# Kernel tuning notes

Measured on AMD Instinct MI355X. Metric: run time of the kernel, lower is better.

The kernel has to match this reference:

```python
import jax, jax.numpy as jnp
import numpy as np

# ---- hyperparameters (from init_kwargs) ----
B, SEQ, D_MODEL = 2, 2048, 1024
D_STATE, D_CONV, EXPAND, HEAD_DIM, CHUNK = 128, 4, 2, 64, 256
D_INNER = EXPAND * D_MODEL            # 2048
NH = D_INNER // HEAD_DIM              # 32 heads
CONV_DIM = D_INNER + 2 * D_STATE      # 2304
D_IN_PROJ = 2 * D_INNER + 2 * D_STATE + NH  # z, xBC, dt -> 4384
D_FF = 4 * D_MODEL
EPS = 1e-12


def setup_inputs() -> dict:
    key = jax.random.key(0)
    ks = jax.random.split(key, 16)
    s = 0.02
    f32 = jnp.float32
    inp = {
        "x": jax.random.normal(ks[0], (B, SEQ, D_MODEL), f32),
        "time_diff": jax.random.uniform(ks[1], (B, SEQ), f32),
        # TiSSD (Mamba2-style) params
        "W_in": jax.random.normal(ks[2], (D_MODEL, D_IN_PROJ), f32) * s,
        "b_in": jnp.zeros((D_IN_PROJ,), f32),
        "conv_w": jax.random.normal(ks[3], (CONV_DIM, D_CONV), f32) * s,
        "conv_b": jnp.zeros((CONV_DIM,), f32),
        "A_log": jnp.log(jnp.arange(1, NH + 1, dtype=f32)),
        "dt_bias": jnp.full((NH,), -2.0, f32),
        "D": jnp.ones((NH,), f32),
        "time_decay": jnp.full((NH,), -3.0, f32),   # time-aware decay rates
        "rms_w": jnp.ones((D_INNER,), f32),
        "W_out": jax.random.normal(ks[4], (D_INNER, D_MODEL), f32) * s,
        "b_out": jnp.zeros((D_MODEL,), f32),
        # wrapper LayerNorm
        "ln_g": jnp.ones((D_MODEL,), f32),
        "ln_b": jnp.zeros((D_MODEL,), f32),
        # FFN
        "fc1_w": jax.random.normal(ks[5], (D_MODEL, D_FF), f32) * s,
        "fc1_b": jnp.zeros((D_FF,), f32),
        "fc2_w": jax.random.normal(ks[6], (D_FF, D_MODEL), f32) * s,
        "fc2_b": jnp.zeros((D_MODEL,), f32),
        "ln2_g": jnp.ones((D_MODEL,), f32),
        "ln2_b": jnp.zeros((D_MODEL,), f32),
    }
    return inp


def _layer_norm(x, g, b, eps=EPS):
    mu = jnp.mean(x, axis=-1, keepdims=True)
    var = jnp.mean(jnp.square(x - mu), axis=-1, keepdims=True)
    return (x - mu) * jax.lax.rsqrt(var + eps) * g + b


def _hardswish(x):
    return x * jnp.clip(x + 3.0, 0.0, 6.0) * (1.0 / 6.0)


def _tissd_forward(x, time_diff, W_in, b_in, conv_w, conv_b, A_log, dt_bias, D,
                   time_decay, rms_w, W_out, b_out):
    b, l, _ = x.shape
    zxbcdt = x @ W_in + b_in                       # [b,l,D_IN_PROJ]
    z = zxbcdt[..., :D_INNER]
    xBC = zxbcdt[..., D_INNER:D_INNER + CONV_DIM]
    dt_raw = zxbcdt[..., -NH:]

    # causal depthwise conv1d (small fixed kernel -> unrolled shifts)
    xp = jnp.pad(xBC, ((0, 0), (D_CONV - 1, 0), (0, 0)))
    xBC_c = conv_b
    for k in range(D_CONV):
        xBC_c = xBC_c + xp[:, k:k + l, :] * conv_w[:, k]
    xBC_c = jax.nn.silu(xBC_c)

    xs = xBC_c[..., :D_INNER]
    Bm = xBC_c[..., D_INNER:D_INNER + D_STATE]     # [b,l,n]
    Cm = xBC_c[..., -D_STATE:]                     # [b,l,n]

    dt = jax.nn.softplus(dt_raw + dt_bias)         # [b,l,h]
    A = -jnp.exp(A_log)                            # [h]
    # time-aware: extra decay proportional to time gap
    dA = dt * A - jax.nn.softplus(time_decay) * time_diff[..., None]  # [b,l,h]

    xh = xs.reshape(b, l, NH, HEAD_DIM)
    xdt = xh * dt[..., None]                       # [b,l,h,p]

    nc = l // CHUNK
    xc = xdt.reshape(b, nc, CHUNK, NH, HEAD_DIM)
    Bc = Bm.reshape(b, nc, CHUNK, D_STATE)
    Cc = Cm.reshape(b, nc, CHUNK, D_STATE)
    dAc = dA.reshape(b, nc, CHUNK, NH).transpose(0, 3, 1, 2)  # [b,h,c,L]

    A_cum = jnp.cumsum(dAc, axis=-1)               # [b,h,c,L]
    seg = A_cum[..., :, None] - A_cum[..., None, :]
    mask = jnp.tril(jnp.ones((CHUNK, CHUNK), bool))
    Lmat = jnp.where(mask, jnp.exp(jnp.where(mask, seg, 0.0)), 0.0)  # [b,h,c,L,L]

    # intra-chunk (diagonal block) output
    Y_diag = jnp.einsum("bcln,bcsn,bhcls,bcshp->bclhp", Cc, Bc, Lmat, xc)

    # per-chunk final states
    decay_states = jnp.exp(A_cum[..., -1:] - A_cum)  # [b,h,c,L]
    states = jnp.einsum("bcln,bhcl,bclhp->bchpn", Bc, decay_states, xc)
    chunk_decay = jnp.exp(A_cum[..., -1])            # [b,h,c]

    # inter-chunk recurrence over nc chunks
    states_t = states.transpose(1, 0, 2, 3, 4)       # [c,b,h,p,n]
    decay_t = chunk_decay.transpose(2, 0, 1)         # [c,b,h]

    def step(carry, inp):
        s_c, d_c = inp
        new = carry * d_c[..., None, None] + s_c
        return new, carry                            # emit state BEFORE chunk

    init = jnp.zeros((b, NH, HEAD_DIM, D_STATE), x.dtype)
    _, prev_states = jax.lax.scan(step, init, (states_t, decay_t))
    prev_states = prev_states.transpose(1, 0, 2, 3, 4)  # [b,c,h,p,n]

    state_decay = jnp.exp(A_cum)                     # [b,h,c,L]
    Y_off = jnp.einsum("bcln,bchpn,bhcl->bclhp", Cc, prev_states, state_decay)

    Y = (Y_diag + Y_off).reshape(b, l, NH, HEAD_DIM) + D[None, None, :, None] * xh
    y = Y.reshape(b, l, D_INNER)

    # gated RMSNorm
    y = y * jax.nn.silu(z)
    y = y * jax.lax.rsqrt(jnp.mean(jnp.square(y), axis=-1, keepdims=True) + EPS) * rms_w
    return y @ W_out + b_out


def reference(x, time_diff, W_in, b_in, conv_w, conv_b, A_log, dt_bias, D,
              time_decay, rms_w, W_out, b_out, ln_g, ln_b,
              fc1_w, fc1_b, fc2_w, fc2_b, ln2_g, ln2_b):
    hidden = _tissd_forward(x, time_diff, W_in, b_in, conv_w, conv_b, A_log,
                            dt_bias, D, time_decay, rms_w, W_out, b_out)
    # num_layers > 1 -> residual; dropout is identity in eval mode
    h = _layer_norm(hidden + x, ln_g, ln_b)
    # FFN with Hardswish and residual LayerNorm
    hid = _hardswish(h @ fc1_w + fc1_b)
    hid = hid @ fc2_w + fc2_b
    out = _layer_norm(hid + h, ln2_g, ln2_b)
    return (out, time_diff)
```

## Files before the change

### kernel.cpp

```cpp
#include <hip/hip_runtime.h>

#define BATCH 2
#define SEQL 2048
#define DM 1024
#define DSTATE 128
#define HD 64
#define CHUNK 256
#define DI 2048
#define NHEADS 32
#define CONVD 2304
#define DPROJ 4384
#define DPROJ_PAD 4608
#define DFF 4096
#define NC 8
#define ROWS (BATCH*SEQL)

typedef unsigned short ushort_t;
typedef short bf16x8 __attribute__((ext_vector_type(8)));
typedef float f32x4 __attribute__((ext_vector_type(4)));

__device__ __forceinline__ float softplus_f(float v){
    return (v > 20.f) ? v : log1pf(expf(v));
}
__device__ __forceinline__ float silu_f(float v){
    return v / (1.f + expf(-v));
}
__device__ __forceinline__ ushort_t f2b(float v){
    union { float f; unsigned int u; } x; x.f = v;
    unsigned int r = x.u + 0x7fffu + ((x.u >> 16) & 1u);
    return (ushort_t)(r >> 16);
}
__device__ __forceinline__ float b2f(ushort_t v){
    union { unsigned int u; float f; } x; x.u = ((unsigned int)v) << 16;
    return x.f;
}

template<int ACT, int OUT_BF16, int TN, int NS, int DTX>
__global__ __launch_bounds__(256) void mfma_gemm_k(
    const ushort_t* __restrict__ A, const ushort_t* __restrict__ Bt,
    const float* __restrict__ bias, float* __restrict__ Cf,
    ushort_t* __restrict__ Cb, float* __restrict__ dtaux,
    int M, int N, int K, int ldc)
{
    constexpr int NT = (TN == 128) ? 4 : 2;
    constexpr int BROWS = TN / 4;
    __shared__ ushort_t As[128*64];
    __shared__ ushort_t Bs[TN*64];
    int tid = threadIdx.x;
    int lane = tid & 63, wave = tid >> 6;
    int m0 = blockIdx.y * 128, n0 = blockIdx.x * TN;
    int Ks = K / NS;
    int kb = (NS > 1) ? blockIdx.z * Ks : 0;
    int wave_m = (TN==128) ? (wave >> 1)*64 : (wave & 1)*64;
    int wave_n = (TN==128) ? (wave & 1)*64 : (wave >> 1)*32;
    int lrow = lane >> 3;
    int lcol = ((lane & 7) ^ lrow) * 8;
    const ushort_t* Abase = A  + (size_t)(m0 + wave*32    + lrow)*K + lcol + kb;
    const ushort_t* Bbase = Bt + (size_t)(n0 + wave*BROWS + lrow)*K + lcol + kb;
    ushort_t* AsW = &As[(wave*32)*64];
    ushort_t* BsW = &Bs[(wave*BROWS)*64];
    f32x4 acc[4][NT];
    #pragma unroll
    for (int i=0;i<4;i++)
        #pragma unroll
        for (int j=0;j<NT;j++) acc[i][j] = (f32x4){0.f,0.f,0.f,0.f};
    int lm = lane & 15;
    int quad = lane >> 4;
    for (int k0 = 0; k0 < Ks; k0 += 64){
        #pragma unroll
        for (int j = 0; j < 4; j++)
            __builtin_amdgcn_global_load_lds(
                (const __attribute__((address_space(1))) void*)(Abase + (size_t)(j*8)*K + k0),
                (__attribute__((address_space(3))) void*)(AsW + j*8*64), 16, 0, 0);
        #pragma unroll
        for (int j = 0; j < BROWS/8; j++)
            __builtin_amdgcn_global_load_lds(
                (const __attribute__((address_space(1))) void*)(Bbase + (size_t)(j*8)*K + k0),
                (__attribute__((address_space(3))) void*)(BsW + j*8*64), 16, 0, 0);
        __syncthreads();
        #pragma unroll
        for (int kk = 0; kk < 64; kk += 32){
            int cb = kk >> 3;
            bf16x8 af[4], bfr[NT];
            #pragma unroll
            for (int mt=0; mt<4; mt++)
                af[mt] = *(const bf16x8*)&As[(wave_m + mt*16 + lm)*64 + (((cb + quad) ^ (lm & 7))*8)];
            #pragma unroll
            for (int nt=0; nt<NT; nt++)
                bfr[nt] = *(const bf16x8*)&Bs[(wave_n + nt*16 + lm)*64 + (((cb + quad) ^ (lm & 7))*8)];
            #pragma unroll
            for (int mt=0; mt<4; mt++)
                #pragma unroll
                for (int nt=0; nt<NT; nt++)
                    acc[mt][nt] = __builtin_amdgcn_mfma_f32_16x16x32_bf16(af[mt], bfr[nt], acc[mt][nt], 0, 0, 0);
        }
        __syncthreads();
    }
    float* Cfo = Cf + (size_t)((NS > 1) ? blockIdx.z : 0) * (size_t)M * ldc;
    int addb = (NS == 1) || (blockIdx.z == 0);
    int crow0 = m0 + wave_m + quad * 4;
    int ccol0 = n0 + wave_n + lm;
    #pragma unroll
    for (int mt=0; mt<4; mt++){
        #pragma unroll
        for (int nt=0; nt<NT; nt++){
            int col = ccol0 + nt*16;
            if (col < N){
                float bv = addb ? bias[col] : 0.f;
                #pragma unroll
                for (int r=0; r<4; r++){
                    int row = crow0 + mt*16 + r;
                    float v = acc[mt][nt][r] + bv;
                    if (ACT == 1){
                        float t = fminf(fmaxf(v + 3.f, 0.f), 6.f);
                        v = v * t * (1.f/6.f);
                    }
                    if (OUT_BF16){
                        Cb[(size_t)row*ldc + col] = f2b(v);
                        if (DTX && col >= N - NHEADS)
                            dtaux[(size_t)row*NHEADS + (col - (N - NHEADS))] = v;
                    } else {
                        Cfo[(size_t)row*ldc + col] = v;
                    }
                }
            }
        }
    }
}

template<int ACT>
__global__ __launch_bounds__(512) void gemm256_k(
    const ushort_t* __restrict__ A, const ushort_t* __restrict__ Bt,
    const float* __restrict__ bias, ushort_t* __restrict__ Cb,
    int M, int N, int K, int ldc, int nbx)
{
    __shared__ ushort_t sm[65536];
    const int tid  = threadIdx.x;
    const int lane = tid & 63, wave = tid >> 6;
    const int lm   = lane & 15, quad = lane >> 4;
    const int wm   = wave >> 2, wn = wave & 3;
    const int nwg = gridDim.x;
    const int cpx = nwg >> 3;
    const int swz = (blockIdx.x & 7)*cpx + (blockIdx.x >> 3);
    const int bx = swz % nbx, by = swz / nbx;
    const int m0 = by << 8, n0 = bx << 8;
    const int NT  = K >> 6;
    const int srow = tid >> 2;
    const int scol = (((tid & 3) ^ ((srow >> 1) & 3)) << 3);
    const ushort_t* pA = A  + (size_t)(m0 + srow)*K + scol;
    const ushort_t* pB = Bt + (size_t)(n0 + srow)*K + scol;
    const size_t rstep = (size_t)128 * K;
    const int swz8 = ((quad ^ ((lm >> 1) & 3)) << 3);
    const int aoff = (wm*128 + lm)*32 + swz8;
    const int boff = 16384 + (wn*64 + lm)*32 + swz8;

#define GL(off, src) __builtin_amdgcn_global_load_lds( \
        (const __attribute__((address_space(1))) void*)(src), \
        (__attribute__((address_space(3))) void*)(&sm[off]), 16, 0, 0)

    {
        const int d = wave*512;
        GL(d,                 pA);        GL(d + 4096,          pA + rstep);
        GL(d + 16384,         pB);        GL(d + 16384 + 4096,  pB + rstep);
        GL(d + 8192,          pA + 32);   GL(d + 8192 + 4096,   pA + 32 + rstep);
        GL(d + 24576,         pB + 32);   GL(d + 24576 + 4096,  pB + 32 + rstep);
    }
    asm volatile("s_waitcnt vmcnt(0)" ::: "memory");
    __builtin_amdgcn_sched_barrier(0);
    __builtin_amdgcn_s_barrier();

    f32x4 acc[8][4];
    #pragma unroll
    for (int i = 0; i < 8; i++)
        #pragma unroll
        for (int j = 0; j < 4; j++) acc[i][j] = (f32x4){0.f,0.f,0.f,0.f};

#define MFMA16(MH) \
    __builtin_amdgcn_s_setprio(1); \
    _Pragma("unroll") \
    for (int mt = 0; mt < 4; mt++) \
        _Pragma("unroll") \
        for (int nt = 0; nt < 4; nt++) \
            acc[(MH)*4+mt][nt] = __builtin_amdgcn_mfma_f32_16x16x32_bf16(af[mt], bf[nt], acc[(MH)*4+mt][nt], 0, 0, 0); \
    __builtin_amdgcn_s_setprio(0);

    for (int t = 0; t < NT; ++t){
        const int bo = (t & 1) << 15;
        const int nb = bo ^ 32768;
        const bool stg = (t < NT-1);
        const ushort_t* pAn = pA + (size_t)(t+1)*64;
        const ushort_t* pBn = pB + (size_t)(t+1)*64;
        bf16x8 af[4], bf[4];

        #pragma unroll
        for (int nt = 0; nt < 4; nt++) bf[nt] = *(const bf16x8*)&sm[bo + boff + nt*512];
        #pragma unroll
        for (int mt = 0; mt < 4; mt++) af[mt] = *(const bf16x8*)&sm[bo + aoff + mt*512];
        if (stg){ GL(nb + wave*512, pAn); GL(nb + 4096 + wave*512, pAn + rstep); }
        __builtin_amdgcn_s_barrier();
        asm volatile("s_waitcnt lgkmcnt(0)");
        __builtin_amdgcn_sched_barrier(0);
        MFMA16(0)
        __builtin_amdgcn_s_barrier();

        #pragma unroll
        for (int mt = 0; mt < 4; mt++) af[mt] = *(const bf16x8*)&sm[bo + aoff + 2048 + mt*512];
        if (stg){ GL(nb + 16384 + wave*512, pBn); GL(nb + 16384 + 4096 + wave*512, pBn + rstep); }
        if (stg) asm volatile("s_waitcnt vmcnt(4)" ::: "memory");
        else     asm volatile("s_waitcnt vmcnt(0)" ::: "memory");
        __builtin_amdgcn_sched_barrier(0);
        __builtin_amdgcn_s_barrier();
        asm volatile("s_waitcnt lgkmcnt(0)");
        __builtin_amdgcn_sched_barrier(0);
        MFMA16(1)
        __builtin_amdgcn_s_barrier();

        #pragma unroll
        for (int nt = 0; nt < 4; nt++) bf[nt] = *(const bf16x8*)&sm[bo + 8192 + boff + nt*512];
        #pragma unroll
        for (int mt = 0; mt < 4; mt++) af[mt] = *(const bf16x8*)&sm[bo + 8192 + aoff + 2048 + mt*512];
        if (stg){ GL(nb + 8192 + wave*512, pAn + 32); GL(nb + 8192 + 4096 + wave*512, pAn + 32 + rstep); }
        __builtin_amdgcn_s_barrier();
        asm volatile("s_waitcnt lgkmcnt(0)");
        __builtin_amdgcn_sched_barrier(0);
        MFMA16(1)
        __builtin_amdgcn_s_barrier();

        #pragma unroll
        for (int mt = 0; mt < 4; mt++) af[mt] = *(const bf16x8*)&sm[bo + 8192 + aoff + mt*512];
        if (stg){
            GL(nb + 24576 + wave*512, pBn + 32); GL(nb + 24576 + 4096 + wave*512, pBn + 32 + rstep);
            asm volatile("s_waitcnt vmcnt(4)" ::: "memory");
            __builtin_amdgcn_sched_barrier(0);
        }
        __builtin_amdgcn_s_barrier();
        asm volatile("s_waitcnt lgkmcnt(0)");
        __builtin_amdgcn_sched_barrier(0);
        MFMA16(0)
        __builtin_amdgcn_s_barrier();
    }
#undef MFMA16
#undef GL

    const int crow = m0 + wm*128 + quad*4;
    const int ccol = n0 + wn*64 + lm;
    #pragma unroll
    for (int m8 = 0; m8 < 8; m8++){
        #pragma unroll
        for (int nt = 0; nt < 4; nt++){
            int col = ccol + nt*16;
            float bv = bias[col];
            #pragma unroll
            for (int r = 0; r < 4; r++){
                int row = crow + m8*16 + r;
                float v = acc[m8][nt][r] + bv;
                if (ACT == 1){
                    float tt = fminf(fmaxf(v + 3.f, 0.f), 6.f);
                    v = v * tt * (1.f/6.f);
                }
                Cb[(size_t)row*ldc + col] = f2b(v);
            }
        }
    }
}

__global__ __launch_bounds__(256) void prep_in_k(const float* __restrict__ x,
                                                 ushort_t* __restrict__ x_bf,
                                                 const float* __restrict__ W_in,
                                                 ushort_t* __restrict__ WinT){
    __shared__ ushort_t tile[32][33];
    int bid = blockIdx.x;
    if (bid < 16384){
        int idx = bid*256 + threadIdx.x;
        x_bf[idx] = f2b(x[idx]);
        return;
    }
    int id2 = bid - 16384;
    int n0 = (id2 % 144)*32, k0 = (id2 / 144)*32;
    int tx = threadIdx.x & 31, ty = threadIdx.x >> 5;
    #pragma unroll
    for (int i = 0; i < 4; i++){
        int k = k0 + ty + i*8;
        int n = n0 + tx;
        float v = (n < DPROJ) ? W_in[(size_t)k*DPROJ + n] : 0.f;
        tile[ty + i*8][tx] = f2b(v);
    }
    __syncthreads();
    #pragma unroll
    for (int i = 0; i < 4; i++)
        WinT[(size_t)(n0 + ty + i*8)*DM + k0 + tx] = tile[tx][ty + i*8];
}

__global__ __launch_bounds__(256) void transpose3_k(const float* __restrict__ Wout,
                                                    const float* __restrict__ fc1w,
                                                    const float* __restrict__ fc2w,
                                                    ushort_t* __restrict__ WoutT,
                                                    ushort_t* __restrict__ fc1T,
                                                    ushort_t* __restrict__ fc2T){
    __shared__ ushort_t tile[32][33];
    int bid = blockIdx.x;
    const float* W; ushort_t* Wt; int K, N, gx, id;
    if (bid < 2048){        W = Wout; Wt = WoutT; K = DI;  N = DM;  gx = 32;  id = bid; }
    else if (bid < 6144){   W = fc1w; Wt = fc1T;  K = DM;  N = DFF; gx = 128; id = bid - 2048; }
    else {                  W = fc2w; Wt = fc2T;  K = DFF; N = DM;  gx = 32;  id = bid - 6144; }
    int n0 = (id % gx)*32, k0 = (id / gx)*32;
    int tx = threadIdx.x & 31, ty = threadIdx.x >> 5;
    #pragma unroll
    for (int i = 0; i < 4; i++){
        int k = k0 + ty + i*8;
        int n = n0 + tx;
        tile[ty + i*8][tx] = f2b(W[(size_t)k*N + n]);
    }
    __syncthreads();
    #pragma unroll
    for (int i = 0; i < 4; i++)
        Wt[(size_t)(n0 + ty + i*8)*K + k0 + tx] = tile[tx][ty + i*8];
}

#define CONVBLKS (ROWS*CONVD/256)
__global__ __launch_bounds__(256) void conv_dt_k(const ushort_t* __restrict__ zx,
                                                 const float* __restrict__ conv_w,
                                                 const float* __restrict__ conv_b,
                                                 ushort_t* __restrict__ convb,
                                                 const float* __restrict__ dtaux,
                                                 const float* __restrict__ time_diff,
                                                 const float* __restrict__ A_log,
                                                 const float* __restrict__ dt_bias,
                                                 const float* __restrict__ time_decay,
                                                 float* __restrict__ dtH,
                                                 float* __restrict__ Acum){
    __shared__ float s[CHUNK];
    int bid = blockIdx.x;
    if (bid < CONVBLKS){
        int idx = bid*256 + threadIdx.x;
        int c = idx % CONVD;
        int row = idx / CONVD;
        int t = row & (SEQL-1);
        float acc = conv_b[c];
        #pragma unroll
        for (int k = 0; k < 4; k++){
            int tt = t + k - 3;
            if (tt >= 0)
                acc += b2f(zx[((size_t)(row + k - 3))*DPROJ + DI + c]) * conv_w[c*4 + k];
        }
        convb[idx] = f2b(silu_f(acc));
        return;
    }
    int id2 = bid - CONVBLKS;
    int c = id2 % NC;
    int h = (id2 / NC) % NHEADS;
    int b = id2 / (NC*NHEADS);
    int l = threadIdx.x;
    int t = c*CHUNK + l;
    float dtr = dtaux[((size_t)(b*SEQL + t))*NHEADS + h];
    float dtv = softplus_f(dtr + dt_bias[h]);
    float A = -expf(A_log[h]);
    float dA = dtv*A - softplus_f(time_decay[h]) * time_diff[b*SEQL + t];
    dtH[((size_t)(b*NHEADS + h))*SEQL + t] = dtv;
    s[l] = dA;
    __syncthreads();
    for (int off = 1; off < CHUNK; off <<= 1){
        float v = (l >= off) ? s[l-off] : 0.f;
        __syncthreads();
        s[l] += v;
        __syncthreads();
    }
    Acum[((size_t)(b*NHEADS + h))*SEQL + t] = s[l];
}

__global__ __launch_bounds__(256) void g_mfma_k(const ushort_t* __restrict__ convb,
                                                ushort_t* __restrict__ G){
    __shared__ ushort_t As[64*136];
    __shared__ ushort_t Bs[64*136];
    int bc = blockIdx.z;
    int l0 = blockIdx.y*64, s0 = blockIdx.x*64;
    int tid = threadIdx.x;
    int lane = tid & 63, wave = tid >> 6;
    int lm = lane & 15, quad = lane >> 4;
    const ushort_t* base = convb + (size_t)bc*CHUNK*CONVD;
    #pragma unroll
    for (int i = 0; i < 4; i++){
        int e = tid + i*256;
        int r = e >> 4, k = (e & 15)*8;
        *(bf16x8*)&As[r*136 + k] = *(const bf16x8*)&base[(size_t)(l0+r)*CONVD + DI + DSTATE + k];
        *(bf16x8*)&Bs[r*136 + k] = *(const bf16x8*)&base[(size_t)(s0+r)*CONVD + DI + k];
    }
    __syncthreads();
    f32x4 acc[4];
    #pragma unroll
    for (int j=0;j<4;j++) acc[j] = (f32x4){0.f,0.f,0.f,0.f};
    #pragma unroll
    for (int kk = 0; kk < 4; kk++){
        bf16x8 af = *(const bf16x8*)&As[(wave*16+lm)*136 + kk*32 + quad*8];
        #pragma unroll
        for (int nt = 0; nt < 4; nt++){
            bf16x8 bfr = *(const bf16x8*)&Bs[(nt*16+lm)*136 + kk*32 + quad*8];
            acc[nt] = __builtin_amdgcn_mfma_f32_16x16x32_bf16(af, bfr, acc[nt], 0, 0, 0);
        }
    }
    ushort_t* g = G + (size_t)bc*CHUNK*CHUNK;
    #pragma unroll
    for (int nt = 0; nt < 4; nt++)
        #pragma unroll
        for (int r = 0; r < 4; r++)
            g[(size_t)(l0 + wave*16 + quad*4 + r)*CHUNK + s0 + nt*16 + lm] = f2b(acc[nt][r]);
}

#define RSX 264
#define RSB 72
__global__ __launch_bounds__(256) void states_mfma_k(const ushort_t* __restrict__ convb,
                                                     const float* __restrict__ dtH,
                                                     const float* __restrict__ Acum,
                                                     float* __restrict__ states){
    __shared__ ushort_t xw[64*RSX];
    __shared__ ushort_t Bt[128*RSB];
    __shared__ float Acs[CHUNK];
    __shared__ float dts[CHUNK];
    int bid = blockIdx.x;
    int h = bid % NHEADS;
    int c = (bid / NHEADS) % NC;
    int b = bid / (NHEADS*NC);
    int tid = threadIdx.x;
    int lane = tid & 63, wave = tid >> 6;
    int lm = lane & 15, quad = lane >> 4;
    Acs[tid] = Acum[((size_t)(b*NHEADS + h))*SEQL + c*CHUNK + tid];
    dts[tid] = dtH[((size_t)(b*NHEADS + h))*SEQL + c*CHUNK + tid];
    __syncthreads();
    float AcL = Acs[CHUNK-1];
    {
        const ushort_t* xg = convb + ((size_t)(b*SEQL + c*CHUNK))*CONVD + h*HD;
        #pragma unroll
        for (int j8 = 0; j8 < 8; j8++){
            int s0 = wave*64 + j8*8;
            bf16x8 pk;
            #pragma unroll
            for (int j = 0; j < 8; j++){
                int l = s0 + j;
                pk[j] = (short)f2b(expf(AcL - Acs[l]) * dts[l] * b2f(xg[(size_t)l*CONVD + lane]));
            }
            *(bf16x8*)&xw[lane*RSX + s0] = pk;
        }
    }
    f32x4 acc[8];
    #pragma unroll
    for (int j=0;j<8;j++) acc[j] = (f32x4){0.f,0.f,0.f,0.f};
    const ushort_t* bbase = convb + ((size_t)(b*SEQL + c*CHUNK))*CONVD + DI;
    for (int l0 = 0; l0 < CHUNK; l0 += 64){
        __syncthreads();
        #pragma unroll
        for (int i = 0; i < 32; i++){
            int e = tid + i*256; int l = e >> 7, n = e & 127;
            Bt[n*RSB + l] = bbase[(size_t)(l0+l)*CONVD + n];
        }
        __syncthreads();
        #pragma unroll
        for (int kk = 0; kk < 2; kk++){
            bf16x8 af = *(const bf16x8*)&xw[(wave*16+lm)*RSX + l0 + kk*32 + quad*8];
            #pragma unroll
            for (int nt = 0; nt < 8; nt++){
                bf16x8 bfr = *(const bf16x8*)&Bt[(nt*16+lm)*RSB + kk*32 + quad*8];
                acc[nt] = __builtin_amdgcn_mfma_f32_16x16x32_bf16(af, bfr, acc[nt], 0, 0, 0);
            }
        }
    }
    float* outp = states + ((size_t)((b*NC + c)*NHEADS + h))*(HD*DSTATE);
    #pragma unroll
    for (int nt = 0; nt < 8; nt++)
        #pragma unroll
        for (int r = 0; r < 4; r++)
            outp[(size_t)(wave*16 + quad*4 + r)*DSTATE + nt*16 + lm] = acc[nt][r];
}

__global__ __launch_bounds__(256) void prev_scan_k(const float* __restrict__ states,
                                                   const float* __restrict__ Acum,
                                                   float* __restrict__ prev){
    int bid = blockIdx.x;
    int part = bid & 15;
    int h = (bid >> 4) & (NHEADS-1);
    int b = bid >> 9;
    int tid = threadIdx.x;
    const float* AcB = Acum + ((size_t)(b*NHEADS + h))*SEQL;
    float dec[NC];
    #pragma unroll
    for (int c = 0; c < NC; c++) dec[c] = expf(AcB[c*CHUNK + CHUNK-1]);
    #pragma unroll
    for (int j = 0; j < 2; j++){
        int e = part*512 + j*256 + tid;
        float carry = 0.f;
        #pragma unroll
        for (int c = 0; c < NC; c++){
            size_t idx = ((size_t)((b*NC + c)*NHEADS + h))*(HD*DSTATE) + e;
            prev[idx] = carry;
            carry = carry*dec[c] + states[idx];
        }
    }
}

#define RLX 264
#define RLP 136
__global__ __launch_bounds__(256) void y_mfma_k(const ushort_t* __restrict__ convb,
                                                const ushort_t* __restrict__ G,
                                                const float* __restrict__ Acum,
                                                const float* __restrict__ dtH,
                                                const float* __restrict__ prev,
                                                const float* __restrict__ Dp,
                                                ushort_t* __restrict__ Ybf){
    __shared__ ushort_t xdtT[64*RLX];
    __shared__ ushort_t prevs[64*RLP];
    __shared__ float Acs[CHUNK];
    __shared__ float dts[CHUNK];
    int bid = blockIdx.x;
    int h = bid % NHEADS;
    int c = (bid / NHEADS) % NC;
    int b = bid / (NHEADS*NC);
    int tid = threadIdx.x;
    int lane = tid & 63, wave = tid >> 6;
    int lm = lane & 15, quad = lane >> 4;

    Acs[tid] = Acum[((size_t)(b*NHEADS + h))*SEQL + c*CHUNK + tid];
    dts[tid] = dtH[((size_t)(b*NHEADS + h))*SEQL + c*CHUNK + tid];
    {
        const float* pv = prev + ((size_t)((b*NC + c)*NHEADS + h))*(HD*DSTATE);
        #pragma unroll
        for (int i = 0; i < 32; i++){
            int e = tid + i*256; int p = e >> 7, n = e & 127;
            prevs[p*RLP + n] = f2b(pv[e]);
        }
    }
    __syncthreads();
    {
        const ushort_t* xg = convb + ((size_t)(b*SEQL + c*CHUNK))*CONVD + h*HD;
        #pragma unroll
        for (int j8 = 0; j8 < 8; j8++){
            int s0 = wave*64 + j8*8;
            bf16x8 pk;
            #pragma unroll
            for (int j = 0; j < 8; j++){
                int l = s0 + j;
                pk[j] = (short)f2b(b2f(xg[(size_t)l*CONVD + lane]) * dts[l]);
            }
            *(bf16x8*)&xdtT[lane*RLX + s0] = pk;
        }
    }
    __syncthreads();

    int   lrow[4];  float Alr[4], eAlr[4];
    #pragma unroll
    for (int mt = 0; mt < 4; mt++){
        lrow[mt] = (mt*4 + wave)*16 + lm;
        Alr[mt]  = Acs[lrow[mt]];
        eAlr[mt] = expf(Alr[mt]);
    }
    const ushort_t* Gbase = G + ((size_t)(b*NC + c))*(CHUNK*CHUNK);

    f32x4 acc[4][4];
    #pragma unroll
    for (int i=0;i<4;i++)
        #pragma unroll
        for (int j=0;j<4;j++) acc[i][j] = (f32x4){0.f,0.f,0.f,0.f};

    for (int ks = 0; ks < 8; ks++){
        bf16x8 bfr[4];
        #pragma unroll
        for (int nt = 0; nt < 4; nt++)
            bfr[nt] = *(const bf16x8*)&xdtT[(nt*16+lm)*RLX + ks*32 + quad*8];
        #pragma unroll
        for (int mt = 0; mt < 4; mt++){
            int rblk = mt*4 + wave;
            int nst = rblk/2 + 1;
            if (ks < nst){
                int sbase = ks*32 + quad*8;
                bf16x8 g8 = *(const bf16x8*)&Gbase[(size_t)lrow[mt]*CHUNK + sbase];
                const float4* A4 = (const float4*)(&Acs[sbase]);
                float4 a0 = A4[0], a1 = A4[1];
                float Al = Alr[mt]; int l = lrow[mt];
                float pv[8];
                pv[0] = (sbase+0 <= l) ? b2f((ushort_t)g8[0])*expf(Al - a0.x) : 0.f;
                pv[1] = (sbase+1 <= l) ? b2f((ushort_t)g8[1])*expf(Al - a0.y) : 0.f;
                pv[2] = (sbase+2 <= l) ? b2f((ushort_t)g8[2])*expf(Al - a0.z) : 0.f;
                pv[3] = (sbase+3 <= l) ? b2f((ushort_t)g8[3])*expf(Al - a0.w) : 0.f;
                pv[4] = (sbase+4 <= l) ? b2f((ushort_t)g8[4])*expf(Al - a1.x) : 0.f;
                pv[5] = (sbase+5 <= l) ? b2f((ushort_t)g8[5])*expf(Al - a1.y) : 0.f;
                pv[6] = (sbase+6 <= l) ? b2f((ushort_t)g8[6])*expf(Al - a1.z) : 0.f;
                pv[7] = (sbase+7 <= l) ? b2f((ushort_t)g8[7])*expf(Al - a1.w) : 0.f;
                bf16x8 af;
                #pragma unroll
                for (int j = 0; j < 8; j++) af[j] = (short)f2b(pv[j]);
                #pragma unroll
                for (int nt = 0; nt < 4; nt++)
                    acc[mt][nt] = __builtin_amdgcn_mfma_f32_16x16x32_bf16(af, bfr[nt], acc[mt][nt], 0, 0, 0);
            }
        }
    }
    for (int kc = 0; kc < 4; kc++){
        bf16x8 bfr[4];
        #pragma unroll
        for (int nt = 0; nt < 4; nt++)
            bfr[nt] = *(const bf16x8*)&prevs[(nt*16+lm)*RLP + kc*32 + quad*8];
        #pragma unroll
        for (int mt = 0; mt < 4; mt++){
            int rowg = b*SEQL + c*CHUNK + lrow[mt];
            bf16x8 c8 = *(const bf16x8*)&convb[(size_t)rowg*CONVD + DI + DSTATE + kc*32 + quad*8];
            float e = eAlr[mt];
            bf16x8 af;
            #pragma unroll
            for (int j = 0; j < 8; j++) af[j] = (short)f2b(e * b2f((ushort_t)c8[j]));
            #pragma unroll
            for (int nt = 0; nt < 4; nt++)
                acc[mt][nt] = __builtin_amdgcn_mfma_f32_16x16x32_bf16(af, bfr[nt], acc[mt][nt], 0, 0, 0);
        }
    }
    float Dv = Dp[h];
    #pragma unroll
    for (int mt = 0; mt < 4; mt++){
        int l0 = (mt*4 + wave)*16 + quad*4;
        #pragma unroll
        for (int nt = 0; nt < 4; nt++){
            int p = nt*16 + lm;
            #pragma unroll
            for (int r = 0; r < 4; r++){
                int rowg = b*SEQL + c*CHUNK + l0 + r;
                float xs = b2f(convb[(size_t)rowg*CONVD + h*HD + p]);
                Ybf[(size_t)rowg*DI + h*HD + p] = f2b(acc[mt][nt][r] + Dv*xs);
            }
        }
    }
}

__global__ __launch_bounds__(256) void gate_rms_k(const ushort_t* __restrict__ Yb,
                                                  const ushort_t* __restrict__ zx,
                                                  const float* __restrict__ rms_w,
                                                  ushort_t* __restrict__ yn){
    __shared__ float red[4];
    __shared__ float scale_s;
    int row = blockIdx.x; int tid = threadIdx.x;
    float v[8]; float ss = 0.f;
    #pragma unroll
    for (int i = 0; i < 8; i++){
        int d = tid + i*256;
        float g = b2f(Yb[(size_t)row*DI + d]) * silu_f(b2f(zx[(size_t)row*DPROJ + d]));
        v[i] = g; ss += g*g;
    }
    #pragma unroll
    for (int off = 32; off > 0; off >>= 1) ss += __shfl_down(ss, off);
    int lane = tid & 63, wid = tid >> 6;
    if (lane == 0) red[wid] = ss;
    __syncthreads();
    if (tid == 0) scale_s = rsqrtf((red[0]+red[1]+red[2]+red[3])*(1.f/DI) + 1e-12f);
    __syncthreads();
    float sc = scale_s;
    #pragma unroll
    for (int i = 0; i < 8; i++){
        int d = tid + i*256;
        yn[(size_t)row*DI + d] = f2b(v[i]*sc*rms_w[d]);
    }
}

__global__ __launch_bounds__(256) void ln_hbf_k(const float* __restrict__ a,
                                                const float* __restrict__ a2,
                                                const float* __restrict__ resid,
                                                const float* __restrict__ g,
                                                const float* __restrict__ bw,
                                                ushort_t* __restrict__ bfout){
    __shared__ float redA[4], redB[4];
    __shared__ float mu_s, rs_s;
    int row = blockIdx.x; int tid = threadIdx.x;
    float u[4]; float s = 0.f, s2 = 0.f;
    #pragma unroll
    for (int i = 0; i < 4; i++){
        int d = tid + i*256;
        float val = a[(size_t)row*DM + d] + a2[(size_t)row*DM + d] + resid[(size_t)row*DM + d];
        u[i] = val; s += val; s2 += val*val;
    }
    #pragma unroll
    for (int off = 32; off > 0; off >>= 1){
        s  += __shfl_down(s,  off);
        s2 += __shfl_down(s2, off);
    }
    int lane = tid & 63, wid = tid >> 6;
    if (lane == 0){ redA[wid] = s; redB[wid] = s2; }
    __syncthreads();
    if (tid == 0){
        float S  = redA[0]+redA[1]+redA[2]+redA[3];
        float S2 = redB[0]+redB[1]+redB[2]+redB[3];
        float mu = S*(1.f/DM);
        float var = S2*(1.f/DM) - mu*mu;
        mu_s = mu; rs_s = rsqrtf(var + 1e-12f);
    }
    __syncthreads();
    float mu = mu_s, rs = rs_s;
    #pragma unroll
    for (int i = 0; i < 4; i++){
        int d = tid + i*256;
        bfout[(size_t)row*DM + d] = f2b((u[i]-mu)*rs*g[d] + bw[d]);
    }
}

__global__ __launch_bounds__(256) void ln_final_k(const float* __restrict__ a,
                                                  const float* __restrict__ a2,
                                                  const ushort_t* __restrict__ residb,
                                                  const float* __restrict__ g,
                                                  const float* __restrict__ bw,
                                                  float* __restrict__ outp,
                                                  const float* __restrict__ td){
    __shared__ float redA[4], redB[4];
    __shared__ float mu_s, rs_s;
    int row = blockIdx.x; int tid = threadIdx.x;
    if (row >= ROWS){
        int idx = (row - ROWS)*256 + tid;
        outp[(size_t)ROWS*DM + idx] = td[idx];
        return;
    }
    float u[4]; float s = 0.f, s2 = 0.f;
    #pragma unroll
    for (int i = 0; i < 4; i++){
        int d = tid + i*256;
        float val = a[(size_t)row*DM + d] + a2[(size_t)row*DM + d] + b2f(residb[(size_t)row*DM + d]);
        u[i] = val; s += val; s2 += val*val;
    }
    #pragma unroll
    for (int off = 32; off > 0; off >>= 1){
        s  += __shfl_down(s,  off);
        s2 += __shfl_down(s2, off);
    }
    int lane = tid & 63, wid = tid >> 6;
    if (lane == 0){ redA[wid] = s; redB[wid] = s2; }
    __syncthreads();
    if (tid == 0){
        float S  = redA[0]+redA[1]+redA[2]+redA[3];
        float S2 = redB[0]+redB[1]+redB[2]+redB[3];
        float mu = S*(1.f/DM);
        float var = S2*(1.f/DM) - mu*mu;
        mu_s = mu; rs_s = rsqrtf(var + 1e-12f);
    }
    __syncthreads();
    float mu = mu_s, rs = rs_s;
    #pragma unroll
    for (int i = 0; i < 4; i++){
        int d = tid + i*256;
        outp[(size_t)row*DM + d] = (u[i]-mu)*rs*g[d] + bw[d];
    }
}

extern "C" void kernel_launch(void* const* d_in, const int* in_sizes, int n_in,
                              void* d_out, int out_size, void* d_ws, size_t ws_size,
                              hipStream_t stream){
    const float* x         = (const float*)d_in[0];
    const float* time_diff = (const float*)d_in[1];
    const float* W_in      = (const float*)d_in[2];
    const float* b_in      = (const float*)d_in[3];
    const float* conv_w    = (const float*)d_in[4];
    const float* conv_b    = (const float*)d_in[5];
    const float* A_log     = (const float*)d_in[6];
    const float* dt_bias   = (const float*)d_in[7];
    const float* Dp        = (const float*)d_in[8];
    const float* time_dec  = (const float*)d_in[9];
    const float* rms_w     = (const float*)d_in[10];
    const float* W_out     = (const float*)d_in[11];
    const float* b_out     = (const float*)d_in[12];
    const float* ln_g      = (const float*)d_in[13];
    const float* ln_b      = (const float*)d_in[14];
    const float* fc1_w     = (const float*)d_in[15];
    const float* fc1_b     = (const float*)d_in[16];
    const float* fc2_w     = (const float*)d_in[17];
    const float* fc2_b     = (const float*)d_in[18];
    const float* ln2_g     = (const float*)d_in[19];
    const float* ln2_b     = (const float*)d_in[20];

    float* ws = (float*)d_ws;
    float* zx    = ws;
    float* convb = zx    + 17956864;
    float* dtH   = convb + 9437184;
    float* Acum  = dtH   + 131072;
    float* r4    = Acum  + 131072;
    float* r5    = r4    + 8388608;
    float* ybreg = r5    + 9437184;
    ushort_t* zx_bf  = (ushort_t*)zx;
    float*    dtaux  = zx + 10600000;
    ushort_t* mid_bf = (ushort_t*)zx;
    ushort_t* h_bf   = (ushort_t*)(zx + 8388608);
    ushort_t* convb_bf = (ushort_t*)convb;
    float* outPa  = convb;
    ushort_t* x_bf  = (ushort_t*)r4;
    ushort_t* WinT  = (ushort_t*)(r4 + 2097152);
    ushort_t* WoutT = (ushort_t*)(r4 + 4194304);
    float* fc2Pa = r4;
    ushort_t* Gb   = (ushort_t*)r5;
    float* stat = r5 + 1048576;
    float* prev = stat + 4194304;
    ushort_t* yn_bf = (ushort_t*)r5;
    ushort_t* fc1T  = (ushort_t*)(r5 + 4194304);
    ushort_t* fc2T  = (ushort_t*)(r5 + 6291456);
    ushort_t* Ybf = (ushort_t*)ybreg;
    float* outp   = (float*)d_out;

    prep_in_k<<<16384 + 4608, 256, 0, stream>>>(x, x_bf, W_in, WinT);
    gemm256_k<0><<<256, 512, 0, stream>>>(x_bf, WinT, b_in, zx_bf,
                                          ROWS, 4096, DM, DPROJ, 16);
    mfma_gemm_k<0,1,128,1,1><<<dim3(3, ROWS/128), 256, 0, stream>>>(
        x_bf, WinT + (size_t)4096*DM, b_in + 4096, nullptr,
        zx_bf + 4096, dtaux, ROWS, 288, DM, DPROJ);
    conv_dt_k<<<CONVBLKS + BATCH*NHEADS*NC, 256, 0, stream>>>(zx_bf, conv_w, conv_b, convb_bf,
                                                              dtaux, time_diff, A_log, dt_bias, time_dec, dtH, Acum);
    g_mfma_k<<<dim3(4,4,BATCH*NC), 256, 0, stream>>>(convb_bf, Gb);
    states_mfma_k<<<BATCH*NC*NHEADS, 256, 0, stream>>>(convb_bf, dtH, Acum, stat);
    prev_scan_k<<<BATCH*NHEADS*16, 256, 0, stream>>>(stat, Acum, prev);
    y_mfma_k<<<BATCH*NC*NHEADS, 256, 0, stream>>>(convb_bf, Gb, Acum, dtH, prev, Dp, Ybf);
    gate_rms_k<<<ROWS, 256, 0, stream>>>(Ybf, zx_bf, rms_w, yn_bf);
    transpose3_k<<<10240, 256, 0, stream>>>(W_out, fc1_w, fc2_w, WoutT, fc1T, fc2T);
    mfma_gemm_k<0,0,64,2,0><<<dim3(DM/64, ROWS/128, 2), 256, 0, stream>>>(yn_bf, WoutT, b_out, outPa, nullptr, nullptr, ROWS, DM, DI, DM);
    ln_hbf_k<<<ROWS, 256, 0, stream>>>(outPa, outPa + (size_t)ROWS*DM, x, ln_g, ln_b, h_bf);
    gemm256_k<1><<<256, 512, 0, stream>>>(h_bf, fc1T, fc1_b, mid_bf,
                                          ROWS, DFF, DM, DFF, 16);
    mfma_gemm_k<0,0,64,2,0><<<dim3(DM/64, ROWS/128, 2), 256, 0, stream>>>(mid_bf, fc2T, fc2_b, fc2Pa, nullptr, nullptr, ROWS, DM, DFF, DM);
    ln_final_k<<<ROWS + ROWS/256, 256, 0, stream>>>(fc2Pa, fc2Pa + (size_t)ROWS*DM, h_bf, ln2_g, ln2_b, outp, time_diff);
}
```

Measured before the change: 518.9 us.

## Vectorize conv and cast kernels, merge in-proj GEMMs, swizzle GEMM block order

Several independent changes land together. The x-to-bf16 cast and the depthwise conv now load and store 4 or 8 elements per thread with vector types. The states kernel precomputes the per-position exp(decay)*dt scale once into shared memory. The two input-projection GEMM launches (gemm256 on the first 4096 columns plus the mfma_gemm tail) become a single mfma_gemm launch over all 4384 columns. That single GEMM also gets an XCD-aware block-index swizzle. Launch count and memory traffic should drop, at the cost of giving up the specialised 256-tile GEMM for the bulk of the in-projection and possibly writing the padded columns.

```diff
diff --git a/kernel.cpp b/kernel.cpp
--- a/kernel.cpp
+++ b/kernel.cpp
@@ -17,6 +17,7 @@
 
 typedef unsigned short ushort_t;
 typedef short bf16x8 __attribute__((ext_vector_type(8)));
+typedef short bf16x4 __attribute__((ext_vector_type(4)));
 typedef float f32x4 __attribute__((ext_vector_type(4)));
 
 __device__ __forceinline__ float softplus_f(float v){
@@ -48,7 +49,11 @@
     __shared__ ushort_t Bs[TN*64];
     int tid = threadIdx.x;
     int lane = tid & 63, wave = tid >> 6;
-    int m0 = blockIdx.y * 128, n0 = blockIdx.x * TN;
+    int gx = gridDim.x;
+    int nb = gx * gridDim.y;
+    int id = blockIdx.x + gx * blockIdx.y;
+    int ids = ((nb & 7) == 0) ? ((id & 7) * (nb >> 3) + (id >> 3)) : id;
+    int m0 = (ids / gx) * 128, n0 = (ids % gx) * TN;
     int Ks = K / NS;
     int kb = (NS > 1) ? blockIdx.z * Ks : 0;
     int wave_m = (TN==128) ? (wave >> 1)*64 : (wave & 1)*64;
@@ -270,12 +275,16 @@
                                                  ushort_t* __restrict__ WinT){
     __shared__ ushort_t tile[32][33];
     int bid = blockIdx.x;
-    if (bid < 16384){
-        int idx = bid*256 + threadIdx.x;
-        x_bf[idx] = f2b(x[idx]);
+    if (bid < 4096){
+        int idx = (bid*256 + threadIdx.x)*4;
+        float4 v = *(const float4*)&x[idx];
+        bf16x4 o;
+        o[0] = (short)f2b(v.x); o[1] = (short)f2b(v.y);
+        o[2] = (short)f2b(v.z); o[3] = (short)f2b(v.w);
+        *(bf16x4*)&x_bf[idx] = o;
         return;
     }
-    int id2 = bid - 16384;
+    int id2 = bid - 4096;
     int n0 = (id2 % 144)*32, k0 = (id2 / 144)*32;
     int tx = threadIdx.x & 31, ty = threadIdx.x >> 5;
     #pragma unroll
@@ -317,7 +326,7 @@
         Wt[(size_t)(n0 + ty + i*8)*K + k0 + tx] = tile[tx][ty + i*8];
 }
 
-#define CONVBLKS (ROWS*CONVD/256)
+#define CONVBLKS8 (ROWS*CONVD/(256*8))
 __global__ __launch_bounds__(256) void conv_dt_k(const ushort_t* __restrict__ zx,
                                                  const float* __restrict__ conv_w,
                                                  const float* __restrict__ conv_b,
@@ -331,22 +340,36 @@
                                                  float* __restrict__ Acum){
     __shared__ float s[CHUNK];
     int bid = blockIdx.x;
-    if (bid < CONVBLKS){
-        int idx = bid*256 + threadIdx.x;
+    if (bid < CONVBLKS8){
+        int idx = (bid*256 + threadIdx.x)*8;
         int c = idx % CONVD;
         int row = idx / CONVD;
         int t = row & (SEQL-1);
-        float acc = conv_b[c];
+        bf16x8 vk[4];
+        bool ok[4];
         #pragma unroll
         for (int k = 0; k < 4; k++){
             int tt = t + k - 3;
-            if (tt >= 0)
-                acc += b2f(zx[((size_t)(row + k - 3))*DPROJ + DI + c]) * conv_w[c*4 + k];
-        }
-        convb[idx] = f2b(silu_f(acc));
+            ok[k] = (tt >= 0);
+            if (ok[k])
+                vk[k] = *(const bf16x8*)&zx[((size_t)(row + k - 3))*DPROJ + DI + c];
+        }
+        const float4* cw = (const float4*)&conv_w[c*4];
+        bf16x8 o;
+        #pragma unroll
+        for (int j = 0; j < 8; j++){
+            float a = conv_b[c + j];
+            float4 w = cw[j];
+            if (ok[0]) a += b2f((ushort_t)vk[0][j]) * w.x;
+            if (ok[1]) a += b2f((ushort_t)vk[1][j]) * w.y;
+            if (ok[2]) a += b2f((ushort_t)vk[2][j]) * w.z;
+            if (ok[3]) a += b2f((ushort_t)vk[3][j]) * w.w;
+            o[j] = (short)f2b(silu_f(a));
+        }
+        *(bf16x8*)&convb[idx] = o;
         return;
     }
-    int id2 = bid - CONVBLKS;
+    int id2 = bid - CONVBLKS8;
     int c = id2 % NC;
     int h = (id2 / NC) % NHEADS;
     int b = id2 / (NC*NHEADS);
@@ -415,7 +438,7 @@
     __shared__ ushort_t xw[64*RSX];
     __shared__ ushort_t Bt[128*RSB];
     __shared__ float Acs[CHUNK];
-    __shared__ float dts[CHUNK];
+    __shared__ float esc[CHUNK];
     int bid = blockIdx.x;
     int h = bid % NHEADS;
     int c = (bid / NHEADS) % NC;
@@ -424,9 +447,10 @@
     int lane = tid & 63, wave = tid >> 6;
     int lm = lane & 15, quad = lane >> 4;
     Acs[tid] = Acum[((size_t)(b*NHEADS + h))*SEQL + c*CHUNK + tid];
-    dts[tid] = dtH[((size_t)(b*NHEADS + h))*SEQL + c*CHUNK + tid];
-    __syncthreads();
-    float AcL = Acs[CHUNK-1];
+    float dtv = dtH[((size_t)(b*NHEADS + h))*SEQL + c*CHUNK + tid];
+    __syncthreads();
+    esc[tid] = expf(Acs[CHUNK-1] - Acs[tid]) * dtv;
+    __syncthreads();
     {
         const ushort_t* xg = convb + ((size_t)(b*SEQL + c*CHUNK))*CONVD + h*HD;
         #pragma unroll
@@ -436,7 +460,7 @@
             #pragma unroll
             for (int j = 0; j < 8; j++){
                 int l = s0 + j;
-                pk[j] = (short)f2b(expf(AcL - Acs[l]) * dts[l] * b2f(xg[(size_t)l*CONVD + lane]));
+                pk[j] = (short)f2b(esc[l] * b2f(xg[(size_t)l*CONVD + lane]));
             }
             *(bf16x8*)&xw[lane*RSX + s0] = pk;
         }
@@ -794,14 +818,11 @@
     ushort_t* Ybf = (ushort_t*)ybreg;
     float* outp   = (float*)d_out;
 
-    prep_in_k<<<16384 + 4608, 256, 0, stream>>>(x, x_bf, W_in, WinT);
-    gemm256_k<0><<<256, 512, 0, stream>>>(x_bf, WinT, b_in, zx_bf,
-                                          ROWS, 4096, DM, DPROJ, 16);
-    mfma_gemm_k<0,1,128,1,1><<<dim3(3, ROWS/128), 256, 0, stream>>>(
-        x_bf, WinT + (size_t)4096*DM, b_in + 4096, nullptr,
-        zx_bf + 4096, dtaux, ROWS, 288, DM, DPROJ);
-    conv_dt_k<<<CONVBLKS + BATCH*NHEADS*NC, 256, 0, stream>>>(zx_bf, conv_w, conv_b, convb_bf,
-                                                              dtaux, time_diff, A_log, dt_bias, time_dec, dtH, Acum);
+    prep_in_k<<<4096 + 4608, 256, 0, stream>>>(x, x_bf, W_in, WinT);
+    mfma_gemm_k<0,1,128,1,1><<<dim3(35, ROWS/128), 256, 0, stream>>>(
+        x_bf, WinT, b_in, nullptr, zx_bf, dtaux, ROWS, DPROJ, DM, DPROJ);
+    conv_dt_k<<<CONVBLKS8 + BATCH*NHEADS*NC, 256, 0, stream>>>(zx_bf, conv_w, conv_b, convb_bf,
+                                                               dtaux, time_diff, A_log, dt_bias, time_dec, dtH, Acum);
     g_mfma_k<<<dim3(4,4,BATCH*NC), 256, 0, stream>>>(convb_bf, Gb);
     states_mfma_k<<<BATCH*NC*NHEADS, 256, 0, stream>>>(convb_bf, dtH, Acum, stat);
     prev_scan_k<<<BATCH*NHEADS*16, 256, 0, stream>>>(stat, Acum, prev);
```

New measurement: 462.2 us. 1.12x faster.
